# Kernel optimization log

Hardware: AMD Instinct MI355X
Metric: run time of the kernel (lower is better)

## Reference

```python
import jax, jax.numpy as jnp
import numpy as np

B, C, H, W = 8, 512, 64, 64
CI = 256  # inter_channels = channel_in // 2
EPS = 1e-5  # BatchNorm eps


def conv1x1(x, w, b):
    # x: (b, c, h, w), w: (o, c), b: (o,)
    return jnp.einsum('bchw,oc->bohw', x, w) + b[None, :, None, None]


def maxpool2(x):
    b, c, h, w = x.shape
    return x.reshape(b, c, h // 2, 2, w // 2, 2).max(axis=(3, 5))


def setup_inputs() -> dict:
    key = jax.random.key(0)
    ks = jax.random.split(key, 13)
    s = 1.0 / np.sqrt(C)
    si = 1.0 / np.sqrt(CI)
    return {
        'x': jax.random.normal(ks[0], (B, C, H, W), dtype=jnp.float32),
        'w_g': jax.random.normal(ks[1], (CI, C), dtype=jnp.float32) * s,
        'b_g': jax.random.normal(ks[2], (CI,), dtype=jnp.float32) * 0.01,
        'w_theta': jax.random.normal(ks[3], (CI, C), dtype=jnp.float32) * s,
        'b_theta': jax.random.normal(ks[4], (CI,), dtype=jnp.float32) * 0.01,
        'w_phi': jax.random.normal(ks[5], (CI, C), dtype=jnp.float32) * s,
        'b_phi': jax.random.normal(ks[6], (CI,), dtype=jnp.float32) * 0.01,
        'w_out': jax.random.normal(ks[7], (C, CI), dtype=jnp.float32) * si,
        'b_out': jax.random.normal(ks[8], (C,), dtype=jnp.float32) * 0.01,
        'bn_gamma': jax.random.normal(ks[9], (C,), dtype=jnp.float32) * 0.1 + 1.0,
        'bn_beta': jax.random.normal(ks[10], (C,), dtype=jnp.float32) * 0.01,
        'bn_mean': jax.random.normal(ks[11], (C,), dtype=jnp.float32) * 0.01,
        'bn_var': jax.random.uniform(ks[12], (C,), dtype=jnp.float32, minval=0.5, maxval=1.5),
    }


def reference(x, w_g, b_g, w_theta, b_theta, w_phi, b_phi,
              w_out, b_out, bn_gamma, bn_beta, bn_mean, bn_var):
    b = x.shape[0]
    # g, phi: 1x1 conv then 2x2 maxpool (sub_sample=True)
    g_x = maxpool2(conv1x1(x, w_g, b_g)).reshape(b, CI, -1)        # (b, ci, M)
    phi_x = maxpool2(conv1x1(x, w_phi, b_phi)).reshape(b, CI, -1)  # (b, ci, M)
    theta_x = conv1x1(x, w_theta, b_theta).reshape(b, CI, -1)      # (b, ci, N)
    # f[b, n, m] = theta^T @ phi  -> softmax over m -> @ g^T
    f = jnp.einsum('bcn,bcm->bnm', theta_x, phi_x)                 # (b, N, M)
    attn = jax.nn.softmax(f, axis=-1)
    y = jnp.einsum('bnm,bcm->bcn', attn, g_x).reshape(b, CI, H, W)
    # W: 1x1 conv + BatchNorm (eval mode, running stats)
    w_y = conv1x1(y, w_out, b_out)
    inv = bn_gamma / jnp.sqrt(bn_var + EPS)
    w_y = w_y * inv[None, :, None, None] + (bn_beta - bn_mean * inv)[None, :, None, None]
    return w_y + x
```

## Files before the change

### kernel.cpp

```cpp
#include <hip/hip_runtime.h>

typedef _Float16 v8h __attribute__((ext_vector_type(8)));
typedef _Float16 v4h __attribute__((ext_vector_type(4)));
typedef float v4f __attribute__((ext_vector_type(4)));
#define HF _Float16

#define Bn 8
#define Cc 512
#define CI 256
#define HW 4096
#define Mp 1024

__device__ __forceinline__ void gload16(const void* g, void* l) {
    __builtin_amdgcn_global_load_lds((const __attribute__((address_space(1))) void*)g,
                                     (__attribute__((address_space(3))) void*)l, 16, 0, 0);
}

__global__ __launch_bounds__(256) void prep_kernel(
    const float* __restrict__ w_g, const float* __restrict__ b_g,
    const float* __restrict__ w_th, const float* __restrict__ b_th,
    const float* __restrict__ w_ph, const float* __restrict__ b_ph,
    const float* __restrict__ w_out, const float* __restrict__ b_out,
    const float* __restrict__ gamma, const float* __restrict__ beta,
    const float* __restrict__ mean, const float* __restrict__ var,
    HF* __restrict__ wall, float* __restrict__ ball,
    HF* __restrict__ wo, float* __restrict__ scale, float* __restrict__ shift)
{
    int idx = blockIdx.x * 256 + threadIdx.x;
    if (idx < 768*512) {
        int o = idx >> 9;
        float v = (o < 256) ? w_th[idx] : (o < 512) ? w_ph[idx - 256*512] : w_g[idx - 512*512];
        wall[idx] = (HF)v;
    }
    if (idx < 512*256) wo[idx] = (HF)w_out[idx];
    if (idx < 768) ball[idx] = (idx < 256) ? b_th[idx] : (idx < 512) ? b_ph[idx-256] : b_g[idx-512];
    if (idx < 512) {
        float inv = gamma[idx] * rsqrtf(var[idx] + 1e-5f);
        scale[idx] = inv;
        shift[idx] = (b_out[idx] - mean[idx]) * inv + beta[idx];
    }
}

__global__ __launch_bounds__(256) void transpose_x_kernel(const float* __restrict__ x, HF* __restrict__ xT)
{
    __shared__ float tile[64][65];
    int b = blockIdx.z;
    int c0 = blockIdx.y * 64, s0 = blockIdx.x * 64;
    int tr = threadIdx.x >> 6, ts = threadIdx.x & 63;
    #pragma unroll
    for (int i = 0; i < 16; ++i) {
        int r = tr + i*4;
        tile[r][ts] = x[((long)(b*Cc) + c0 + r)*HW + s0 + ts];
    }
    __syncthreads();
    #pragma unroll
    for (int i = 0; i < 16; ++i) {
        int r = tr + i*4;
        xT[((long)b*HW + s0 + r)*Cc + c0 + ts] = (HF)tile[ts][r];
    }
}

__global__ __launch_bounds__(256) void pool_sm_kernel(const HF* __restrict__ TP, HF* __restrict__ Pt)
{
    int idx = blockIdx.x * 256 + threadIdx.x;
    int c8 = idx & 31;
    int m  = (idx >> 5) & 1023;
    int b  = idx >> 15;
    int h2 = m >> 5, w2 = m & 31;
    int s00 = h2*128 + w2*2;
    const HF* base = TP + ((long)b*HW + s00)*512 + 256 + c8*8;
    v8h a0 = *(const v8h*)(base);
    v8h a1 = *(const v8h*)(base + 512);
    v8h a2 = *(const v8h*)(base + 64*512);
    v8h a3 = *(const v8h*)(base + 65*512);
    v8h o;
    #pragma unroll
    for (int j = 0; j < 8; ++j) {
        float v = fmaxf(fmaxf((float)a0[j], (float)a1[j]), fmaxf((float)a2[j], (float)a3[j]));
        o[j] = (HF)v;
    }
    *(v8h*)(Pt + ((long)b*Mp + m)*CI + c8*8) = o;
}

__global__ __launch_bounds__(256) void pool_kernel(const HF* __restrict__ src, long sSrc,
                                                   HF* __restrict__ dst, long sDst)
{
    long idx = (long)blockIdx.x * 256 + threadIdx.x;
    int m = idx & 1023;
    long bc = idx >> 10;
    int c = (int)(bc & 255);
    int b = (int)(bc >> 8);
    int h2 = m >> 5, w2 = m & 31;
    const HF* p = src + (long)b*sSrc + (long)c*HW + h2*128 + w2*2;
    float v = fmaxf(fmaxf((float)p[0], (float)p[1]), fmaxf((float)p[64], (float)p[65]));
    dst[(long)b*sDst + (long)c*Mp + m] = (HF)v;
}

template<int EPI>
__global__ __launch_bounds__(256) void gemm_bt_kernel(
    const HF* __restrict__ A, long sA, const HF* __restrict__ B, long sB,
    void* __restrict__ Cv, long sC, int M, int N, int K,
    const float* __restrict__ bias,
    const float* __restrict__ rowScale, const float* __restrict__ rowShift,
    const float* __restrict__ Xres, long sX)
{
    __shared__ HF As[128][40];
    __shared__ HF Bs[128][40];
    int b = blockIdx.z;
    int i0 = blockIdx.y * 128;
    int j0 = blockIdx.x * 128;
    const HF* Ab = A + (long)b * sA;
    const HF* Bb = B + (long)b * sB;
    int tid = threadIdx.x;
    int lane = tid & 63, w = tid >> 6;
    int wr = w >> 1, wc = w & 1;
    int lr = lane & 15, lk = (lane >> 4) * 8;

    v4f acc[4][4];
    #pragma unroll
    for (int i = 0; i < 4; ++i)
        #pragma unroll
        for (int j = 0; j < 4; ++j) { v4f z = {0.f,0.f,0.f,0.f}; acc[i][j] = z; }

    for (int k0 = 0; k0 < K; k0 += 32) {
        #pragma unroll
        for (int q = 0; q < 2; ++q) {
            int ch = tid*2 + q;
            int row = ch >> 2;
            int c8 = (ch & 3) * 8;
            const uint4* ga = (const uint4*)(Ab + (long)(i0+row)*K + k0 + c8);
            *(uint4*)(&As[row][c8]) = *ga;
            const uint4* gb = (const uint4*)(Bb + (long)(j0+row)*K + k0 + c8);
            *(uint4*)(&Bs[row][c8]) = *gb;
        }
        __syncthreads();
        v8h af[4], bfr[4];
        #pragma unroll
        for (int mf = 0; mf < 4; ++mf)
            af[mf] = *(const v8h*)(&As[wr*64 + mf*16 + lr][lk]);
        #pragma unroll
        for (int nf = 0; nf < 4; ++nf)
            bfr[nf] = *(const v8h*)(&Bs[wc*64 + nf*16 + lr][lk]);
        #pragma unroll
        for (int mf = 0; mf < 4; ++mf)
            #pragma unroll
            for (int nf = 0; nf < 4; ++nf)
                acc[mf][nf] = __builtin_amdgcn_mfma_f32_16x16x32_f16(af[mf], bfr[nf], acc[mf][nf], 0, 0, 0);
        __syncthreads();
    }

    int rbase = (lane >> 4) * 4;
    #pragma unroll
    for (int mf = 0; mf < 4; ++mf) {
        #pragma unroll
        for (int nf = 0; nf < 4; ++nf) {
            #pragma unroll
            for (int r = 0; r < 4; ++r) {
                int row = i0 + wr*64 + mf*16 + rbase + r;
                int col = j0 + wc*64 + nf*16 + lr;
                float v = acc[mf][nf][r];
                if (EPI == 0) {
                    v += bias[row];
                    ((HF*)Cv + (long)b*sC)[(long)row*N + col] = (HF)v;
                } else if (EPI == 3) {
                    v += bias[col];
                    ((HF*)Cv + (long)b*sC)[(long)row*N + col] = (HF)v;
                } else {
                    float* Cf = (float*)Cv + (long)b*sC;
                    const float* Xb = Xres + (long)b*sX;
                    long o = (long)row*N + col;
                    Cf[o] = v * rowScale[row] + rowShift[row] + Xb[o];
                }
            }
        }
    }
}

__global__ __launch_bounds__(256, 2) void fused_attn_kernel(
    const HF* __restrict__ TP,
    const HF* __restrict__ Pt,
    const HF* __restrict__ G,
    HF* __restrict__ Yt)
{
    __shared__ alignas(16) HF P_lds[2][8192];
    __shared__ alignas(16) HF P_buf[2][4][16][36];
    __shared__ alignas(16) float smem_a[2][4][16];
    __shared__ float smem_l[64];

    int bid = blockIdx.x;
    int b = bid & 7;
    int ntile = bid >> 3;
    int tid = threadIdx.x;
    int lane = tid & 63, w = tid >> 6;
    int lr = lane & 15, lkg = lane >> 4;
    int nbase = ntile * 64;

    const HF* Tq = TP + ((long)b*HW + nbase + w*16) * 512;
    const HF* Pb = Pt + (long)b*Mp*CI;
    const HF* Gb = G  + (long)b*CI*Mp + (long)(w*64)*Mp;

    auto stage = [&](int bsel, int m0) {
        #pragma unroll
        for (int q = 0; q < 4; ++q) {
            int idxp = (w*4 + q)*64 + lane;
            int pkg = idxp >> 5, prow = idxp & 31;
            gload16(Pb + (long)(m0 + prow)*CI + pkg*8, P_lds[bsel] + (size_t)idxp*8);
        }
    };
    auto loadG = [&](int m0, v8h* g) {
        #pragma unroll
        for (int ct = 0; ct < 4; ++ct)
            g[ct] = *(const v8h*)(Gb + (long)(ct*16 + lr)*Mp + m0 + lkg*8);
    };

    v8h af[8];
    #pragma unroll
    for (int kf = 0; kf < 8; ++kf)
        af[kf] = *(const v8h*)(Tq + (long)lr*512 + kf*32 + lkg*8);

    v4f acc_y[4][4];
    #pragma unroll
    for (int i = 0; i < 4; ++i)
        #pragma unroll
        for (int j = 0; j < 4; ++j) { v4f z = {0.f,0.f,0.f,0.f}; acc_y[i][j] = z; }
    float mrun = -1e30f;
    float lsum = 0.f;

    v8h gA[4], gB[4];
    stage(0, 0);
    loadG(0, gA);
    __syncthreads();

    for (int t = 0; t < 32; ++t) {
        int cur = t & 1;
        int pb = t & 1;
        v8h* gcur  = (t & 1) ? gB : gA;
        v8h* gnext = (t & 1) ? gA : gB;
        if (t < 31) {
            stage(cur ^ 1, (t+1)*32);
            loadG((t+1)*32, gnext);
        }

        v4f acc[2];
        #pragma unroll
        for (int mt = 0; mt < 2; ++mt) { v4f z = {0.f,0.f,0.f,0.f}; acc[mt] = z; }
        __builtin_amdgcn_s_setprio(1);
        #pragma unroll
        for (int kf = 0; kf < 8; ++kf) {
            #pragma unroll
            for (int mt = 0; mt < 2; ++mt) {
                v8h pf = *(const v8h*)(P_lds[cur] + (kf*4 + lkg)*256 + (mt*16 + lr)*8);
                acc[mt] = __builtin_amdgcn_mfma_f32_16x16x32_f16(pf, af[kf], acc[mt], 0, 0, 0);
            }
        }
        __builtin_amdgcn_s_setprio(0);

        float cm = fmaxf(fmaxf(fmaxf(acc[0][0], acc[0][1]), fmaxf(acc[0][2], acc[0][3])),
                         fmaxf(fmaxf(acc[1][0], acc[1][1]), fmaxf(acc[1][2], acc[1][3])));
        cm = fmaxf(cm, __shfl_xor(cm, 16));
        cm = fmaxf(cm, __shfl_xor(cm, 32));
        float alpha = 1.f;
        if (cm > mrun + 7.f) {
            alpha = __expf(mrun - cm);
            mrun = cm;
            lsum *= alpha;
        }
        if (lane < 16) smem_a[pb][w][lr] = alpha;
        #pragma unroll
        for (int mt = 0; mt < 2; ++mt) {
            v4h p4;
            #pragma unroll
            for (int r = 0; r < 4; ++r) {
                float p = __expf(acc[mt][r] - mrun);
                lsum += p;
                p4[r] = (HF)p;
            }
            *(v4h*)(&P_buf[pb][w][lr][mt*16 + lkg*4]) = p4;
        }

        __syncthreads();

        __builtin_amdgcn_s_setprio(1);
        v4f alv[4];
        bool need = false;
        #pragma unroll
        for (int rt = 0; rt < 4; ++rt) {
            alv[rt] = *(const v4f*)(&smem_a[pb][rt][lkg*4]);
            need = need | (alv[rt][0] != 1.f) | (alv[rt][1] != 1.f)
                        | (alv[rt][2] != 1.f) | (alv[rt][3] != 1.f);
        }
        if (__any(need)) {
            #pragma unroll
            for (int rt = 0; rt < 4; ++rt)
                #pragma unroll
                for (int ct = 0; ct < 4; ++ct)
                    #pragma unroll
                    for (int r = 0; r < 4; ++r)
                        acc_y[rt][ct][r] *= alv[rt][r];
        }
        #pragma unroll
        for (int rt = 0; rt < 4; ++rt) {
            v8h ap;
            {
                v4h a0 = *(const v4h*)(&P_buf[pb][rt][lr][lkg*8]);
                v4h a1 = *(const v4h*)(&P_buf[pb][rt][lr][lkg*8 + 4]);
                ap = __builtin_shufflevector(a0, a1, 0,1,2,3,4,5,6,7);
            }
            #pragma unroll
            for (int ct = 0; ct < 4; ++ct)
                acc_y[rt][ct] = __builtin_amdgcn_mfma_f32_16x16x32_f16(ap, gcur[ct], acc_y[rt][ct], 0, 0, 0);
        }
        __builtin_amdgcn_s_setprio(0);
    }

    lsum += __shfl_xor(lsum, 16);
    lsum += __shfl_xor(lsum, 32);
    if (lane < 16) smem_l[w*16 + lr] = lsum;
    __syncthreads();
    HF* Yb = Yt + ((long)b*HW + nbase) * CI;
    #pragma unroll
    for (int rt = 0; rt < 4; ++rt) {
        #pragma unroll
        for (int r = 0; r < 4; ++r) {
            int row = rt*16 + lkg*4 + r;
            float inv = 1.f / smem_l[row];
            #pragma unroll
            for (int ct = 0; ct < 4; ++ct)
                Yb[(long)row*CI + w*64 + ct*16 + lr] = (HF)(acc_y[rt][ct][r] * inv);
        }
    }
}

extern "C" void kernel_launch(void* const* d_in, const int* in_sizes, int n_in,
                              void* d_out, int out_size, void* d_ws, size_t ws_size,
                              hipStream_t stream)
{
    const float* x     = (const float*)d_in[0];
    const float* w_g   = (const float*)d_in[1];
    const float* b_g   = (const float*)d_in[2];
    const float* w_th  = (const float*)d_in[3];
    const float* b_th  = (const float*)d_in[4];
    const float* w_ph  = (const float*)d_in[5];
    const float* b_ph  = (const float*)d_in[6];
    const float* w_out = (const float*)d_in[7];
    const float* b_out = (const float*)d_in[8];
    const float* gamma = (const float*)d_in[9];
    const float* beta  = (const float*)d_in[10];
    const float* mean  = (const float*)d_in[11];
    const float* var   = (const float*)d_in[12];
    float* out = (float*)d_out;

    char* ws = (char*)d_ws;
    size_t off = 0;
    auto alloc = [&](size_t bytes) { void* p = ws + off; off += (bytes + 255) & ~(size_t)255; return p; };
    HF*    wall  = (HF*)alloc((size_t)768*512*2);
    float* ball  = (float*)alloc(768*4);
    HF*    wo    = (HF*)alloc((size_t)512*256*2);
    float* scale = (float*)alloc(512*4);
    float* shift = (float*)alloc(512*4);
    HF*    xT    = (HF*)alloc((size_t)Bn*HW*Cc*2);
    HF*    TP    = (HF*)alloc((size_t)Bn*HW*512*2);
    HF*    Gg    = (HF*)alloc((size_t)Bn*CI*HW*2);
    HF*    Pt    = (HF*)alloc((size_t)Bn*Mp*CI*2);
    HF*    G     = (HF*)alloc((size_t)Bn*CI*Mp*2);
    HF*    Yt    = (HF*)alloc((size_t)Bn*HW*CI*2);

    prep_kernel<<<1536, 256, 0, stream>>>(w_g,b_g,w_th,b_th,w_ph,b_ph,w_out,b_out,gamma,beta,mean,var,
                                          wall, ball, wo, scale, shift);
    transpose_x_kernel<<<dim3(64,8,Bn), 256, 0, stream>>>(x, xT);
    gemm_bt_kernel<3><<<dim3(4,32,Bn), 256, 0, stream>>>(xT, (long)HW*Cc, wall, 0, TP, (long)HW*512,
                                                         HW, 512, Cc, ball, nullptr, nullptr, nullptr, 0);
    gemm_bt_kernel<0><<<dim3(32,2,Bn), 256, 0, stream>>>(wall + (size_t)512*512, 0, xT, (long)HW*Cc,
                                                         Gg, (long)CI*HW, CI, HW, Cc, ball + 512,
                                                         nullptr, nullptr, nullptr, 0);
    pool_sm_kernel<<<1024, 256, 0, stream>>>(TP, Pt);
    pool_kernel<<<8192, 256, 0, stream>>>(Gg, (long)CI*HW, G, (long)CI*Mp);
    fused_attn_kernel<<<512, 256, 0, stream>>>(TP, Pt, G, Yt);
    gemm_bt_kernel<2><<<dim3(32,4,Bn), 256, 0, stream>>>(wo, 0, Yt, (long)HW*CI, out, (long)Cc*HW,
                                                         Cc, HW, CI, nullptr, scale, shift, x, (long)Cc*HW);
}
```

Baseline: 201.1 us.

## Split attention waves into producer (QK+softmax) and consumer (PV) roles with software pipelining

The fused attention kernel now gives its four waves two roles. Two producer waves each compute QK^T scores and the softmax numerators for 32 query rows. Two consumer waves each accumulate P·G for 128 of the 256 output channels, one tile behind the producers, through double-buffered LDS. This is meant to overlap the exp/softmax work with the PV MFMAs across waves, where before every wave ran both phases in sequence. In exchange it adds an extra loop iteration, doubles the per-wave register load (af[2][8], acc_y[4][8], gA/gB[8]), and creates a load imbalance between the two roles that may limit occupancy under launch_bounds(256,2).

```diff
diff --git a/kernel.cpp b/kernel.cpp
--- a/kernel.cpp
+++ b/kernel.cpp
@@ -183,8 +183,8 @@
     HF* __restrict__ Yt)
 {
     __shared__ alignas(16) HF P_lds[2][8192];
-    __shared__ alignas(16) HF P_buf[2][4][16][36];
-    __shared__ alignas(16) float smem_a[2][4][16];
+    __shared__ alignas(16) HF P_buf[2][64][36];
+    __shared__ alignas(16) float smem_a[2][64];
     __shared__ float smem_l[64];
 
     int bid = blockIdx.x;
@@ -194,139 +194,169 @@
     int lane = tid & 63, w = tid >> 6;
     int lr = lane & 15, lkg = lane >> 4;
     int nbase = ntile * 64;
-
-    const HF* Tq = TP + ((long)b*HW + nbase + w*16) * 512;
+    bool producer = (w < 2);
+
     const HF* Pb = Pt + (long)b*Mp*CI;
-    const HF* Gb = G  + (long)b*CI*Mp + (long)(w*64)*Mp;
+
+    int prow0 = w * 32;
+    const HF* Tq = TP + ((long)b*HW + nbase + prow0) * 512;
+    v8h af[2][8];
+    float mrun[2] = {-1e30f, -1e30f};
+    float lsum[2] = {0.f, 0.f};
+
+    int chalf = (w - 2) * 128;
+    const HF* Gb = G + (long)b*CI*Mp + (long)chalf*Mp;
+    v4f acc_y[4][8];
+    v8h gA[8], gB[8];
 
     auto stage = [&](int bsel, int m0) {
         #pragma unroll
-        for (int q = 0; q < 4; ++q) {
-            int idxp = (w*4 + q)*64 + lane;
+        for (int q = 0; q < 8; ++q) {
+            int idxp = (w*8 + q)*64 + lane;
             int pkg = idxp >> 5, prow = idxp & 31;
             gload16(Pb + (long)(m0 + prow)*CI + pkg*8, P_lds[bsel] + (size_t)idxp*8);
         }
     };
     auto loadG = [&](int m0, v8h* g) {
         #pragma unroll
-        for (int ct = 0; ct < 4; ++ct)
+        for (int ct = 0; ct < 8; ++ct)
             g[ct] = *(const v8h*)(Gb + (long)(ct*16 + lr)*Mp + m0 + lkg*8);
     };
 
-    v8h af[8];
-    #pragma unroll
-    for (int kf = 0; kf < 8; ++kf)
-        af[kf] = *(const v8h*)(Tq + (long)lr*512 + kf*32 + lkg*8);
-
-    v4f acc_y[4][4];
-    #pragma unroll
-    for (int i = 0; i < 4; ++i)
-        #pragma unroll
-        for (int j = 0; j < 4; ++j) { v4f z = {0.f,0.f,0.f,0.f}; acc_y[i][j] = z; }
-    float mrun = -1e30f;
-    float lsum = 0.f;
-
-    v8h gA[4], gB[4];
-    stage(0, 0);
-    loadG(0, gA);
+    if (producer) {
+        #pragma unroll
+        for (int nt = 0; nt < 2; ++nt)
+            #pragma unroll
+            for (int kf = 0; kf < 8; ++kf)
+                af[nt][kf] = *(const v8h*)(Tq + (long)(nt*16 + lr)*512 + kf*32 + lkg*8);
+        stage(0, 0);
+    } else {
+        #pragma unroll
+        for (int i = 0; i < 4; ++i)
+            #pragma unroll
+            for (int j = 0; j < 8; ++j) { v4f z = {0.f,0.f,0.f,0.f}; acc_y[i][j] = z; }
+        loadG(0, gA);
+    }
     __syncthreads();
 
-    for (int t = 0; t < 32; ++t) {
-        int cur = t & 1;
-        int pb = t & 1;
-        v8h* gcur  = (t & 1) ? gB : gA;
-        v8h* gnext = (t & 1) ? gA : gB;
-        if (t < 31) {
-            stage(cur ^ 1, (t+1)*32);
-            loadG((t+1)*32, gnext);
-        }
-
-        v4f acc[2];
-        #pragma unroll
-        for (int mt = 0; mt < 2; ++mt) { v4f z = {0.f,0.f,0.f,0.f}; acc[mt] = z; }
-        __builtin_amdgcn_s_setprio(1);
-        #pragma unroll
-        for (int kf = 0; kf < 8; ++kf) {
-            #pragma unroll
-            for (int mt = 0; mt < 2; ++mt) {
-                v8h pf = *(const v8h*)(P_lds[cur] + (kf*4 + lkg)*256 + (mt*16 + lr)*8);
-                acc[mt] = __builtin_amdgcn_mfma_f32_16x16x32_f16(pf, af[kf], acc[mt], 0, 0, 0);
+    #pragma unroll 2
+    for (int t = 0; t <= 32; ++t) {
+        if (producer) {
+            if (t < 32) {
+                int cur = t & 1;
+                if (t < 31) stage(cur ^ 1, (t+1)*32);
+
+                v4f sacc[2][2];
+                #pragma unroll
+                for (int nt = 0; nt < 2; ++nt)
+                    #pragma unroll
+                    for (int mt = 0; mt < 2; ++mt) { v4f z = {0.f,0.f,0.f,0.f}; sacc[nt][mt] = z; }
+                __builtin_amdgcn_s_setprio(1);
+                #pragma unroll
+                for (int kf = 0; kf < 8; ++kf) {
+                    #pragma unroll
+                    for (int mt = 0; mt < 2; ++mt) {
+                        v8h pf = *(const v8h*)(P_lds[cur] + (kf*4 + lkg)*256 + (mt*16 + lr)*8);
+                        sacc[0][mt] = __builtin_amdgcn_mfma_f32_16x16x32_f16(pf, af[0][kf], sacc[0][mt], 0, 0, 0);
+                        sacc[1][mt] = __builtin_amdgcn_mfma_f32_16x16x32_f16(pf, af[1][kf], sacc[1][mt], 0, 0, 0);
+                    }
+                }
+                __builtin_amdgcn_s_setprio(0);
+
+                int pb = t & 1;
+                #pragma unroll
+                for (int nt = 0; nt < 2; ++nt) {
+                    float cm = fmaxf(fmaxf(fmaxf(sacc[nt][0][0], sacc[nt][0][1]),
+                                           fmaxf(sacc[nt][0][2], sacc[nt][0][3])),
+                                     fmaxf(fmaxf(sacc[nt][1][0], sacc[nt][1][1]),
+                                           fmaxf(sacc[nt][1][2], sacc[nt][1][3])));
+                    cm = fmaxf(cm, __shfl_xor(cm, 16));
+                    cm = fmaxf(cm, __shfl_xor(cm, 32));
+                    float alpha = 1.f;
+                    if (cm > mrun[nt] + 7.f) {
+                        alpha = __expf(mrun[nt] - cm);
+                        mrun[nt] = cm;
+                        lsum[nt] *= alpha;
+                    }
+                    int row = prow0 + nt*16 + lr;
+                    if (lkg == 0) smem_a[pb][row] = alpha;
+                    #pragma unroll
+                    for (int mt = 0; mt < 2; ++mt) {
+                        v4h p4;
+                        #pragma unroll
+                        for (int r = 0; r < 4; ++r) {
+                            float p = __expf(sacc[nt][mt][r] - mrun[nt]);
+                            lsum[nt] += p;
+                            p4[r] = (HF)p;
+                        }
+                        *(v4h*)(&P_buf[pb][row][mt*16 + lkg*4]) = p4;
+                    }
+                }
             }
-        }
-        __builtin_amdgcn_s_setprio(0);
-
-        float cm = fmaxf(fmaxf(fmaxf(acc[0][0], acc[0][1]), fmaxf(acc[0][2], acc[0][3])),
-                         fmaxf(fmaxf(acc[1][0], acc[1][1]), fmaxf(acc[1][2], acc[1][3])));
-        cm = fmaxf(cm, __shfl_xor(cm, 16));
-        cm = fmaxf(cm, __shfl_xor(cm, 32));
-        float alpha = 1.f;
-        if (cm > mrun + 7.f) {
-            alpha = __expf(mrun - cm);
-            mrun = cm;
-            lsum *= alpha;
-        }
-        if (lane < 16) smem_a[pb][w][lr] = alpha;
-        #pragma unroll
-        for (int mt = 0; mt < 2; ++mt) {
-            v4h p4;
+        } else {
+            if (t >= 1) {
+                if (t < 32) loadG(t*32, (t & 1) ? gB : gA);
+                int pbc = (t-1) & 1;
+                v8h* gcur = ((t-1) & 1) ? gB : gA;
+
+                v4f alv[4];
+                bool need = false;
+                #pragma unroll
+                for (int rt = 0; rt < 4; ++rt) {
+                    alv[rt] = *(const v4f*)(&smem_a[pbc][rt*16 + lkg*4]);
+                    need = need | (alv[rt][0] != 1.f) | (alv[rt][1] != 1.f)
+                                | (alv[rt][2] != 1.f) | (alv[rt][3] != 1.f);
+                }
+                if (__any(need)) {
+                    #pragma unroll
+                    for (int rt = 0; rt < 4; ++rt)
+                        #pragma unroll
+                        for (int ct = 0; ct < 8; ++ct)
+                            #pragma unroll
+                            for (int r = 0; r < 4; ++r)
+                                acc_y[rt][ct][r] *= alv[rt][r];
+                }
+                __builtin_amdgcn_s_setprio(1);
+                #pragma unroll
+                for (int rt = 0; rt < 4; ++rt) {
+                    v8h ap;
+                    {
+                        v4h a0 = *(const v4h*)(&P_buf[pbc][rt*16 + lr][lkg*8]);
+                        v4h a1 = *(const v4h*)(&P_buf[pbc][rt*16 + lr][lkg*8 + 4]);
+                        ap = __builtin_shufflevector(a0, a1, 0,1,2,3,4,5,6,7);
+                    }
+                    #pragma unroll
+                    for (int ct = 0; ct < 8; ++ct)
+                        acc_y[rt][ct] = __builtin_amdgcn_mfma_f32_16x16x32_f16(ap, gcur[ct], acc_y[rt][ct], 0, 0, 0);
+                }
+                __builtin_amdgcn_s_setprio(0);
+            }
+        }
+        __syncthreads();
+    }
+
+    if (producer) {
+        #pragma unroll
+        for (int nt = 0; nt < 2; ++nt) {
+            float s = lsum[nt];
+            s += __shfl_xor(s, 16);
+            s += __shfl_xor(s, 32);
+            if (lkg == 0) smem_l[prow0 + nt*16 + lr] = s;
+        }
+    }
+    __syncthreads();
+    if (!producer) {
+        HF* Yb = Yt + ((long)b*HW + nbase) * CI + chalf;
+        #pragma unroll
+        for (int rt = 0; rt < 4; ++rt) {
             #pragma unroll
             for (int r = 0; r < 4; ++r) {
-                float p = __expf(acc[mt][r] - mrun);
-                lsum += p;
-                p4[r] = (HF)p;
+                int row = rt*16 + lkg*4 + r;
+                float inv = 1.f / smem_l[row];
+                #pragma unroll
+                for (int ct = 0; ct < 8; ++ct)
+                    Yb[(long)row*CI + ct*16 + lr] = (HF)(acc_y[rt][ct][r] * inv);
             }
-            *(v4h*)(&P_buf[pb][w][lr][mt*16 + lkg*4]) = p4;
-        }
-
-        __syncthreads();
-
-        __builtin_amdgcn_s_setprio(1);
-        v4f alv[4];
-        bool need = false;
-        #pragma unroll
-        for (int rt = 0; rt < 4; ++rt) {
-            alv[rt] = *(const v4f*)(&smem_a[pb][rt][lkg*4]);
-            need = need | (alv[rt][0] != 1.f) | (alv[rt][1] != 1.f)
-                        | (alv[rt][2] != 1.f) | (alv[rt][3] != 1.f);
-        }
-        if (__any(need)) {
-            #pragma unroll
-            for (int rt = 0; rt < 4; ++rt)
-                #pragma unroll
-                for (int ct = 0; ct < 4; ++ct)
-                    #pragma unroll
-                    for (int r = 0; r < 4; ++r)
-                        acc_y[rt][ct][r] *= alv[rt][r];
-        }
-        #pragma unroll
-        for (int rt = 0; rt < 4; ++rt) {
-            v8h ap;
-            {
-                v4h a0 = *(const v4h*)(&P_buf[pb][rt][lr][lkg*8]);
-                v4h a1 = *(const v4h*)(&P_buf[pb][rt][lr][lkg*8 + 4]);
-                ap = __builtin_shufflevector(a0, a1, 0,1,2,3,4,5,6,7);
-            }
-            #pragma unroll
-            for (int ct = 0; ct < 4; ++ct)
-                acc_y[rt][ct] = __builtin_amdgcn_mfma_f32_16x16x32_f16(ap, gcur[ct], acc_y[rt][ct], 0, 0, 0);
-        }
-        __builtin_amdgcn_s_setprio(0);
-    }
-
-    lsum += __shfl_xor(lsum, 16);
-    lsum += __shfl_xor(lsum, 32);
-    if (lane < 16) smem_l[w*16 + lr] = lsum;
-    __syncthreads();
-    HF* Yb = Yt + ((long)b*HW + nbase) * CI;
-    #pragma unroll
-    for (int rt = 0; rt < 4; ++rt) {
-        #pragma unroll
-        for (int r = 0; r < 4; ++r) {
-            int row = rt*16 + lkg*4 + r;
-            float inv = 1.f / smem_l[row];
-            #pragma unroll
-            for (int ct = 0; ct < 4; ++ct)
-                Yb[(long)row*CI + w*64 + ct*16 + lr] = (HF)(acc_y[rt][ct][r] * inv);
         }
     }
 }
```

Result: slower. 287.7 us (+43.1%).

## Fuse output projection, BatchNorm and residual into attention kernel epilogue

Applied to the files above, without the earlier changes.

The attention kernel now keeps the normalized Y tile in LDS and immediately multiplies it by the output 1x1 conv weights with MFMA. It then applies the BN scale/shift and residual add, writing the final fp32 output. This removes the Yt intermediate buffer's global write and read and the separate GEMM launch. It adds LDS usage and a large accumulator set, which may reduce occupancy or cause spills, and the weight fragments are read directly from global memory.

```diff
diff --git a/kernel.cpp b/kernel.cpp
--- a/kernel.cpp
+++ b/kernel.cpp
@@ -180,12 +180,16 @@
     const HF* __restrict__ TP,
     const HF* __restrict__ Pt,
     const HF* __restrict__ G,
-    HF* __restrict__ Yt)
+    const HF* __restrict__ wo,
+    const float* __restrict__ scale, const float* __restrict__ shift,
+    const float* __restrict__ x,
+    float* __restrict__ out)
 {
     __shared__ alignas(16) HF P_lds[2][8192];
     __shared__ alignas(16) HF P_buf[2][4][16][36];
     __shared__ alignas(16) float smem_a[2][4][16];
     __shared__ float smem_l[64];
+    __shared__ alignas(16) HF Y_lds[64][264];
 
     int bid = blockIdx.x;
     int b = bid & 7;
@@ -317,7 +321,6 @@
     lsum += __shfl_xor(lsum, 32);
     if (lane < 16) smem_l[w*16 + lr] = lsum;
     __syncthreads();
-    HF* Yb = Yt + ((long)b*HW + nbase) * CI;
     #pragma unroll
     for (int rt = 0; rt < 4; ++rt) {
         #pragma unroll
@@ -326,7 +329,44 @@
             float inv = 1.f / smem_l[row];
             #pragma unroll
             for (int ct = 0; ct < 4; ++ct)
-                Yb[(long)row*CI + w*64 + ct*16 + lr] = (HF)(acc_y[rt][ct][r] * inv);
+                Y_lds[row][w*64 + ct*16 + lr] = (HF)(acc_y[rt][ct][r] * inv);
+        }
+    }
+    __syncthreads();
+
+    const HF* wob = wo + (long)(w*128)*CI;
+    v4f acc2[8][4];
+    #pragma unroll
+    for (int i = 0; i < 8; ++i)
+        #pragma unroll
+        for (int j = 0; j < 4; ++j) { v4f z = {0.f,0.f,0.f,0.f}; acc2[i][j] = z; }
+    #pragma unroll
+    for (int kf = 0; kf < 8; ++kf) {
+        v8h bf2[4];
+        #pragma unroll
+        for (int nt = 0; nt < 4; ++nt)
+            bf2[nt] = *(const v8h*)(&Y_lds[nt*16 + lr][kf*32 + lkg*8]);
+        #pragma unroll
+        for (int cot = 0; cot < 8; ++cot) {
+            v8h af2 = *(const v8h*)(wob + (long)(cot*16 + lr)*CI + kf*32 + lkg*8);
+            #pragma unroll
+            for (int nt = 0; nt < 4; ++nt)
+                acc2[cot][nt] = __builtin_amdgcn_mfma_f32_16x16x32_f16(af2, bf2[nt], acc2[cot][nt], 0, 0, 0);
+        }
+    }
+    const float* xb = x + (long)b*Cc*HW + nbase;
+    float* ob = out + (long)b*Cc*HW + nbase;
+    #pragma unroll
+    for (int cot = 0; cot < 8; ++cot) {
+        int co = w*128 + cot*16 + lkg*4;
+        #pragma unroll
+        for (int r = 0; r < 4; ++r) {
+            float sc = scale[co + r], sh = shift[co + r];
+            #pragma unroll
+            for (int nt = 0; nt < 4; ++nt) {
+                long o = (long)(co + r)*HW + nt*16 + lr;
+                ob[o] = acc2[cot][nt][r] * sc + sh + xb[o];
+            }
         }
     }
 }
@@ -363,7 +403,6 @@
     HF*    Gg    = (HF*)alloc((size_t)Bn*CI*HW*2);
     HF*    Pt    = (HF*)alloc((size_t)Bn*Mp*CI*2);
     HF*    G     = (HF*)alloc((size_t)Bn*CI*Mp*2);
-    HF*    Yt    = (HF*)alloc((size_t)Bn*HW*CI*2);
 
     prep_kernel<<<1536, 256, 0, stream>>>(w_g,b_g,w_th,b_th,w_ph,b_ph,w_out,b_out,gamma,beta,mean,var,
                                           wall, ball, wo, scale, shift);
@@ -375,7 +414,5 @@
                                                          nullptr, nullptr, nullptr, 0);
     pool_sm_kernel<<<1024, 256, 0, stream>>>(TP, Pt);
     pool_kernel<<<8192, 256, 0, stream>>>(Gg, (long)CI*HW, G, (long)CI*Mp);
-    fused_attn_kernel<<<512, 256, 0, stream>>>(TP, Pt, G, Yt);
-    gemm_bt_kernel<2><<<dim3(32,4,Bn), 256, 0, stream>>>(wo, 0, Yt, (long)HW*CI, out, (long)Cc*HW,
-                                                         Cc, HW, CI, nullptr, scale, shift, x, (long)Cc*HW);
-}
+    fused_attn_kernel<<<512, 256, 0, stream>>>(TP, Pt, G, wo, scale, shift, x, out);
+}
```

Result: faster. 193.0 us (-4.0%).
